# Kernel tuning notes

Measured on AMD Instinct MI355X. Metric: run time of the kernel, lower is better.

Reference implementation:

```python
import jax, jax.numpy as jnp
import numpy as np

G = 60            # 60x60 macroblock MV grid (960px / 16px blocks)
IMAGE_SIZE = 960.0
LN_EPS = 1e-5


def layer_norm(x, g, b):
    mu = jnp.mean(x, -1, keepdims=True)
    var = jnp.var(x, -1, keepdims=True)
    return (x - mu) / jnp.sqrt(var + LN_EPS) * g + b


def setup_inputs() -> dict:
    key = jax.random.key(0)
    ks = iter(jax.random.split(key, 40))
    nk = lambda: next(ks)
    N = 4096
    MVF, BED, H = 64, 32, 128
    D_IN = MVF + BED  # 96

    def lin(out_d, in_d):
        w = jax.random.normal(nk(), (out_d, in_d), jnp.float32) * np.float32(1.0 / np.sqrt(in_d))
        b = jnp.zeros((out_d,), jnp.float32)
        return w, b

    motion_vectors = jax.random.normal(nk(), (1, 2, G, G), jnp.float32)
    xy = jax.random.uniform(nk(), (N, 2), jnp.float32, 0.0, 800.0)
    wh = jax.random.uniform(nk(), (N, 2), jnp.float32, 16.0, 160.0)
    boxes = jnp.concatenate([xy, jnp.clip(xy + wh, 0.0, IMAGE_SIZE)], axis=-1)

    inp = {"motion_vectors": motion_vectors, "boxes": boxes}
    # stats projection: 6 stats (mean/std/range x 2 channels) -> MVF
    inp["W_stats"], inp["b_stats"] = lin(MVF, 6)
    inp["g_stats"] = jnp.ones((MVF,), jnp.float32); inp["be_stats"] = jnp.zeros((MVF,), jnp.float32)
    # box coordinate encoder
    inp["W_b1"], inp["b_b1"] = lin(BED, 4)
    inp["g_b1"] = jnp.ones((BED,), jnp.float32); inp["be_b1"] = jnp.zeros((BED,), jnp.float32)
    inp["W_b2"], inp["b_b2"] = lin(BED, BED)
    inp["g_b2"] = jnp.ones((BED,), jnp.float32); inp["be_b2"] = jnp.zeros((BED,), jnp.float32)
    # single-layer LSTM (torch gate order i,f,g,o)
    inp["W_ih"] = jax.random.normal(nk(), (4 * H, D_IN), jnp.float32) * np.float32(1.0 / np.sqrt(D_IN))
    inp["W_hh"] = jax.random.normal(nk(), (4 * H, H), jnp.float32) * np.float32(1.0 / np.sqrt(H))
    inp["b_ih"] = jnp.zeros((4 * H,), jnp.float32)
    inp["b_hh"] = jnp.zeros((4 * H,), jnp.float32)
    # heads
    inp["W_p1"], inp["b_p1"] = lin(H // 2, H); inp["W_p2"], inp["b_p2"] = lin(2, H // 2)
    inp["W_s1"], inp["b_s1"] = lin(H // 2, H); inp["W_s2"], inp["b_s2"] = lin(2, H // 2)
    inp["W_c1"], inp["b_c1"] = lin(H // 2, H); inp["W_c2"], inp["b_c2"] = lin(1, H // 2)
    return inp


def _box_motion_stats(motion_vectors, boxes_norm):
    # motion_vectors: [1,2,G,G]; boxes_norm: [N,4] in [0,1]
    mvf = motion_vectors[0].reshape(2, G * G)  # [2, 3600]
    x1 = jnp.clip(jnp.floor(boxes_norm[:, 0] * G).astype(jnp.int32), 0, G - 1)
    y1 = jnp.clip(jnp.floor(boxes_norm[:, 1] * G).astype(jnp.int32), 0, G - 1)
    x2 = jnp.clip(jnp.ceil(boxes_norm[:, 2] * G).astype(jnp.int32), x1 + 1, G)
    y2 = jnp.clip(jnp.ceil(boxes_norm[:, 3] * G).astype(jnp.int32), y1 + 1, G)
    idx = jnp.arange(G)
    mx = (idx[None, :] >= x1[:, None]) & (idx[None, :] < x2[:, None])  # [N,G]
    my = (idx[None, :] >= y1[:, None]) & (idx[None, :] < y2[:, None])  # [N,G]
    mask = (my[:, :, None] & mx[:, None, :]).reshape(-1, G * G).astype(mvf.dtype)  # [N,3600]
    cnt = mask.sum(-1, keepdims=True)  # >= 1 by construction
    s = jnp.einsum('nc,kc->nk', mask, mvf)          # [N,2]
    sq = jnp.einsum('nc,kc->nk', mask, mvf * mvf)   # [N,2]
    mean = s / cnt
    std = jnp.sqrt(jnp.clip(sq / cnt - mean * mean, 0.0))
    big = jnp.asarray(1e30, mvf.dtype)
    hi = jnp.where(mask[:, None, :] > 0, mvf[None], -big).max(-1)  # [N,2]
    lo = jnp.where(mask[:, None, :] > 0, mvf[None], big).min(-1)   # [N,2]
    return jnp.concatenate([mean, std, hi - lo], axis=-1)  # [N,6]


def reference(motion_vectors, boxes,
              W_stats, b_stats, g_stats, be_stats,
              W_b1, b_b1, g_b1, be_b1, W_b2, b_b2, g_b2, be_b2,
              W_ih, W_hh, b_ih, b_hh,
              W_p1, b_p1, W_p2, b_p2, W_s1, b_s1, W_s2, b_s2, W_c1, b_c1, W_c2, b_c2):
    N = boxes.shape[0]
    H = W_hh.shape[1]
    boxes_norm = jnp.clip(boxes / IMAGE_SIZE, 0.0, 1.0)

    # per-box motion feature (BoxAlignedMotionEncoder: gather region -> mean/std/range -> proj)
    stats = _box_motion_stats(motion_vectors, boxes_norm)
    mv_feat = jax.nn.relu(layer_norm(stats @ W_stats.T + b_stats, g_stats, be_stats))  # [N,64]

    # box coordinate encoder (dropout = identity in eval)
    h1 = jax.nn.relu(layer_norm(boxes_norm @ W_b1.T + b_b1, g_b1, be_b1))
    box_feat = jax.nn.relu(layer_norm(h1 @ W_b2.T + b_b2, g_b2, be_b2))  # [N,32]

    x = jnp.concatenate([mv_feat, box_feat], axis=-1)  # [N,96]

    # single-step LSTM, zero initial state, torch gate order i,f,g,o
    h0 = jnp.zeros((N, H), x.dtype)
    c0 = jnp.zeros((N, H), x.dtype)
    gates = x @ W_ih.T + h0 @ W_hh.T + b_ih + b_hh
    i, f, g, o = jnp.split(gates, 4, axis=-1)
    c = jax.nn.sigmoid(f) * c0 + jax.nn.sigmoid(i) * jnp.tanh(g)
    h = jax.nn.sigmoid(o) * jnp.tanh(c)  # [N,128]

    pos = jax.nn.relu(h @ W_p1.T + b_p1) @ W_p2.T + b_p2    # [N,2]
    size = jax.nn.relu(h @ W_s1.T + b_s1) @ W_s2.T + b_s2   # [N,2]
    conf = jax.nn.relu(h @ W_c1.T + b_c1) @ W_c2.T + b_c2   # [N,1]
    confidences = jax.nn.sigmoid(conf[:, 0])

    # box update: shift center by deltas, scale w/h by exp(size_deltas)
    x1, y1, x2, y2 = boxes[:, 0], boxes[:, 1], boxes[:, 2], boxes[:, 3]
    cx, cy = (x1 + x2) * 0.5, (y1 + y2) * 0.5
    w, hgt = x2 - x1, y2 - y1
    ncx, ncy = cx + pos[:, 0], cy + pos[:, 1]
    nw, nh = w * jnp.exp(size[:, 0]), hgt * jnp.exp(size[:, 1])
    pred = jnp.stack([ncx - nw * 0.5, ncy - nh * 0.5, ncx + nw * 0.5, ncy + nh * 0.5], axis=-1)
    return jnp.concatenate([pred, confidences[:, None]], axis=-1)  # [N,5]
```

## Files before the change

kernel.cpp:

```cpp
#include <hip/hip_runtime.h>
#include <math.h>

#define GRID_G 60
#define GRID_GG 3600
#define BPB 8

__device__ __forceinline__ float wred32sum(float v){
  #pragma unroll
  for (int m = 16; m; m >>= 1) v += __shfl_xor(v, m, 32);
  return v;
}
__device__ __forceinline__ float wred32max(float v){
  #pragma unroll
  for (int m = 16; m; m >>= 1) v = fmaxf(v, __shfl_xor(v, m, 32));
  return v;
}
__device__ __forceinline__ float wred32min(float v){
  #pragma unroll
  for (int m = 16; m; m >>= 1) v = fminf(v, __shfl_xor(v, m, 32));
  return v;
}
__device__ __forceinline__ float frcp(float x){ return __builtin_amdgcn_rcpf(x); }
__device__ __forceinline__ float fsig(float x){ return frcp(1.0f + __expf(-x)); }
__device__ __forceinline__ float ftanh(float x){ return 1.0f - 2.0f*frcp(1.0f + __expf(2.0f*x)); }

__global__ __launch_bounds__(256) void transpose_kernel(
    const float* __restrict__ W_ih,
    const float* __restrict__ W_p1, const float* __restrict__ W_s1,
    const float* __restrict__ W_c1,
    float* __restrict__ wt_ih, float* __restrict__ wt_h)
{
  const int i4 = blockIdx.x * 256 + threadIdx.x;
  if (i4 < 9216) {
    const int e = i4 * 4;
    const int k = e / 384, r0 = e % 384;
    float4 v;
    {
      const int r = r0;     const int row = (r < 128) ? r : r + 128; v.x = W_ih[row*96 + k];
    }
    { const int r = r0 + 1; const int row = (r < 128) ? r : r + 128; v.y = W_ih[row*96 + k]; }
    { const int r = r0 + 2; const int row = (r < 128) ? r : r + 128; v.z = W_ih[row*96 + k]; }
    { const int r = r0 + 3; const int row = (r < 128) ? r : r + 128; v.w = W_ih[row*96 + k]; }
    ((float4*)wt_ih)[i4] = v;
  } else if (i4 < 9216 + 6144) {
    const int j4 = i4 - 9216;
    const int e = j4 * 4;
    const int k = e / 192, r0 = e % 192;
    const float* W = (r0 < 64) ? W_p1 : (r0 < 128) ? W_s1 : W_c1;
    float4 v;
    v.x = W[((r0    ) & 63) * 128 + k];
    v.y = W[((r0 + 1) & 63) * 128 + k];
    v.z = W[((r0 + 2) & 63) * 128 + k];
    v.w = W[((r0 + 3) & 63) * 128 + k];
    ((float4*)wt_h)[j4] = v;
  }
}

__global__ __launch_bounds__(256) void tracker_kernel(
    const float* __restrict__ mv,
    const float* __restrict__ boxes,
    const float* __restrict__ W_stats, const float* __restrict__ b_stats,
    const float* __restrict__ g_stats, const float* __restrict__ be_stats,
    const float* __restrict__ W_b1,  const float* __restrict__ b_b1,
    const float* __restrict__ g_b1,  const float* __restrict__ be_b1,
    const float* __restrict__ W_b2,  const float* __restrict__ b_b2,
    const float* __restrict__ g_b2,  const float* __restrict__ be_b2,
    const float* __restrict__ wt_ih,
    const float* __restrict__ b_ih,  const float* __restrict__ b_hh,
    const float* __restrict__ wt_h,
    const float* __restrict__ b_p1,  const float* __restrict__ W_p2, const float* __restrict__ b_p2,
    const float* __restrict__ b_s1,  const float* __restrict__ W_s2, const float* __restrict__ b_s2,
    const float* __restrict__ b_c1,  const float* __restrict__ W_c2, const float* __restrict__ b_c2,
    float* __restrict__ out, int N)
{
  __shared__ __align__(16) float x_lds[BPB][96];
  __shared__ __align__(16) float sA[BPB][384];
  __shared__ __align__(16) float sB[BPB][384];
  __shared__ __align__(16) float h_lds[BPB][128];
  __shared__ __align__(16) float h1_lds[BPB][32];
  __shared__ float u_lds[3*BPB][65];
  __shared__ float res_lds[BPB][5];

  const int tid  = threadIdx.x;
  const int base = blockIdx.x * BPB;

  {
    const int b   = tid >> 5;
    const int l32 = tid & 31;
    int gb = base + b; if (gb >= N) gb = N - 1;
    const float4 bx = ((const float4*)boxes)[gb];
    const float bn0 = fminf(fmaxf(bx.x * (1.0f/960.0f), 0.f), 1.f);
    const float bn1 = fminf(fmaxf(bx.y * (1.0f/960.0f), 0.f), 1.f);
    const float bn2 = fminf(fmaxf(bx.z * (1.0f/960.0f), 0.f), 1.f);
    const float bn3 = fminf(fmaxf(bx.w * (1.0f/960.0f), 0.f), 1.f);

    int x1 = (int)floorf(bn0 * 60.f); x1 = min(max(x1, 0), 59);
    int y1 = (int)floorf(bn1 * 60.f); y1 = min(max(y1, 0), 59);
    int x2 = (int)ceilf (bn2 * 60.f); x2 = min(max(x2, x1 + 1), 60);
    int y2 = (int)ceilf (bn3 * 60.f); y2 = min(max(y2, y1 + 1), 60);
    const int w = x2 - x1, hh = y2 - y1;
    const int cnt = w * hh;
    const float rw = 1.0f / (float)w;

    float s0=0.f, s1=0.f, q0=0.f, q1=0.f;
    float hi0=-1e30f, hi1=-1e30f, lo0=1e30f, lo1=1e30f;
    for (int c = l32; c < cnt; c += 32) {
      const int yy = (int)(((float)c + 0.5f) * rw);
      const int xx = c - yy * w;
      const int idx = (y1 + yy) * GRID_G + (x1 + xx);
      const float m0 = mv[idx];
      const float m1 = mv[GRID_GG + idx];
      s0 += m0; q0 += m0*m0; hi0 = fmaxf(hi0, m0); lo0 = fminf(lo0, m0);
      s1 += m1; q1 += m1*m1; hi1 = fmaxf(hi1, m1); lo1 = fminf(lo1, m1);
    }
    s0 = wred32sum(s0); q0 = wred32sum(q0); hi0 = wred32max(hi0); lo0 = wred32min(lo0);
    s1 = wred32sum(s1); q1 = wred32sum(q1); hi1 = wred32max(hi1); lo1 = wred32min(lo1);
    const float inv = frcp((float)cnt);
    float st[6];
    st[0] = s0 * inv;
    st[1] = s1 * inv;
    st[2] = sqrtf(fmaxf(q0 * inv - st[0]*st[0], 0.f));
    st[3] = sqrtf(fmaxf(q1 * inv - st[1]*st[1], 0.f));
    st[4] = hi0 - lo0;
    st[5] = hi1 - lo1;

    {
      const float* Wr0 = W_stats + l32 * 6;
      const float* Wr1 = W_stats + (l32 + 32) * 6;
      float v0 = b_stats[l32], v1 = b_stats[l32 + 32];
      #pragma unroll
      for (int k = 0; k < 6; ++k) { v0 = fmaf(st[k], Wr0[k], v0); v1 = fmaf(st[k], Wr1[k], v1); }
      const float mu  = wred32sum(v0 + v1) * (1.0f/64.0f);
      const float var = wred32sum(v0*v0 + v1*v1) * (1.0f/64.0f) - mu*mu;
      const float rs  = rsqrtf(var + 1e-5f);
      x_lds[b][l32     ] = fmaxf((v0-mu)*rs*g_stats[l32     ] + be_stats[l32     ], 0.f);
      x_lds[b][l32 + 32] = fmaxf((v1-mu)*rs*g_stats[l32 + 32] + be_stats[l32 + 32], 0.f);
    }

    {
      const float* Wr = W_b1 + l32 * 4;
      const float v = b_b1[l32] + bn0*Wr[0] + bn1*Wr[1] + bn2*Wr[2] + bn3*Wr[3];
      const float mu  = wred32sum(v)   * (1.0f/32.0f);
      const float var = wred32sum(v*v) * (1.0f/32.0f) - mu*mu;
      h1_lds[b][l32] = fmaxf((v - mu) * rsqrtf(var + 1e-5f) * g_b1[l32] + be_b1[l32], 0.f);
    }
    __threadfence_block();

    {
      const float* Wr = W_b2 + l32 * 32;
      float v = b_b2[l32];
      #pragma unroll
      for (int kk = 0; kk < 8; ++kk) {
        const float4 hv = *(const float4*)(&h1_lds[b][kk * 4]);
        const float4 wv = *(const float4*)(&Wr[kk * 4]);
        v = fmaf(wv.x,hv.x, fmaf(wv.y,hv.y, fmaf(wv.z,hv.z, fmaf(wv.w,hv.w, v))));
      }
      const float mu  = wred32sum(v)   * (1.0f/32.0f);
      const float var = wred32sum(v*v) * (1.0f/32.0f) - mu*mu;
      x_lds[b][64 + l32] = fmaxf((v - mu) * rsqrtf(var + 1e-5f) * g_b2[l32] + be_b2[l32], 0.f);
    }
  }
  __syncthreads();

  if (tid < 192) {
    const int q = (tid < 96) ? tid : tid - 96;
    const int s = (tid < 96) ? 0 : 1;
    float acc[4][BPB];
    #pragma unroll
    for (int j = 0; j < 4; ++j)
      #pragma unroll
      for (int b = 0; b < BPB; ++b) acc[j][b] = 0.f;
    const float4* WT = (const float4*)wt_ih;
    const int k0 = s * 48;
    #pragma unroll 2
    for (int k4 = 0; k4 < 12; ++k4) {
      const int kb = k0 + 4*k4;
      const float4 wv0 = WT[(size_t)(kb    ) * 96 + q];
      const float4 wv1 = WT[(size_t)(kb + 1) * 96 + q];
      const float4 wv2 = WT[(size_t)(kb + 2) * 96 + q];
      const float4 wv3 = WT[(size_t)(kb + 3) * 96 + q];
      #pragma unroll
      for (int b = 0; b < BPB; ++b) {
        const float4 xv = *(const float4*)(&x_lds[b][kb]);
        acc[0][b] = fmaf(wv0.x, xv.x, fmaf(wv1.x, xv.y, fmaf(wv2.x, xv.z, fmaf(wv3.x, xv.w, acc[0][b]))));
        acc[1][b] = fmaf(wv0.y, xv.x, fmaf(wv1.y, xv.y, fmaf(wv2.y, xv.z, fmaf(wv3.y, xv.w, acc[1][b]))));
        acc[2][b] = fmaf(wv0.z, xv.x, fmaf(wv1.z, xv.y, fmaf(wv2.z, xv.z, fmaf(wv3.z, xv.w, acc[2][b]))));
        acc[3][b] = fmaf(wv0.w, xv.x, fmaf(wv1.w, xv.y, fmaf(wv2.w, xv.z, fmaf(wv3.w, xv.w, acc[3][b]))));
      }
    }
    float* dst = (s == 0) ? &sA[0][0] : &sB[0][0];
    #pragma unroll
    for (int b = 0; b < BPB; ++b) {
      float4 v; v.x = acc[0][b]; v.y = acc[1][b]; v.z = acc[2][b]; v.w = acc[3][b];
      *(float4*)(dst + b * 384 + 4 * q) = v;
    }
  }
  __syncthreads();

  {
    const int j    = tid & 127;
    const int half = tid >> 7;
    const float bi = b_ih[j      ] + b_hh[j      ];
    const float bg = b_ih[j + 256] + b_hh[j + 256];
    const float bo = b_ih[j + 384] + b_hh[j + 384];
    #pragma unroll
    for (int bb = 0; bb < 4; ++bb) {
      const int b = half * 4 + bb;
      const float ai = sA[b][j      ] + sB[b][j      ] + bi;
      const float ag = sA[b][128 + j] + sB[b][128 + j] + bg;
      const float ao = sA[b][256 + j] + sB[b][256 + j] + bo;
      const float c  = fsig(ai) * ftanh(ag);
      h_lds[b][j] = fsig(ao) * ftanh(c);
    }
  }
  __syncthreads();

  if (tid < 192) {
    const int q48 = tid % 48;
    const int s4  = tid / 48;
    float acc[4][BPB];
    #pragma unroll
    for (int j = 0; j < 4; ++j)
      #pragma unroll
      for (int b = 0; b < BPB; ++b) acc[j][b] = 0.f;
    const float4* WT = (const float4*)wt_h;
    const int k0 = s4 * 32;
    #pragma unroll 2
    for (int k4 = 0; k4 < 8; ++k4) {
      const int kb = k0 + 4*k4;
      const float4 wv0 = WT[(size_t)(kb    ) * 48 + q48];
      const float4 wv1 = WT[(size_t)(kb + 1) * 48 + q48];
      const float4 wv2 = WT[(size_t)(kb + 2) * 48 + q48];
      const float4 wv3 = WT[(size_t)(kb + 3) * 48 + q48];
      #pragma unroll
      for (int b = 0; b < BPB; ++b) {
        const float4 hv = *(const float4*)(&h_lds[b][kb]);
        acc[0][b] = fmaf(wv0.x, hv.x, fmaf(wv1.x, hv.y, fmaf(wv2.x, hv.z, fmaf(wv3.x, hv.w, acc[0][b]))));
        acc[1][b] = fmaf(wv0.y, hv.x, fmaf(wv1.y, hv.y, fmaf(wv2.y, hv.z, fmaf(wv3.y, hv.w, acc[1][b]))));
        acc[2][b] = fmaf(wv0.z, hv.x, fmaf(wv1.z, hv.y, fmaf(wv2.z, hv.z, fmaf(wv3.z, hv.w, acc[2][b]))));
        acc[3][b] = fmaf(wv0.w, hv.x, fmaf(wv1.w, hv.y, fmaf(wv2.w, hv.z, fmaf(wv3.w, hv.w, acc[3][b]))));
      }
    }
    float* dst = (s4 < 2) ? &sA[0][0] : &sB[0][0];
    const int off = (s4 & 1) * 192;
    #pragma unroll
    for (int b = 0; b < BPB; ++b) {
      float4 v; v.x = acc[0][b]; v.y = acc[1][b]; v.z = acc[2][b]; v.w = acc[3][b];
      *(float4*)(dst + b * 384 + off + 4 * q48) = v;
    }
  }
  __syncthreads();

  {
    #pragma unroll
    for (int i = 0; i < 6; ++i) {
      const int idx = tid + 256 * i;
      const int b = idx / 192;
      const int r = idx - b * 192;
      const int head = r >> 6, brow = r & 63;
      const float bias = ((head == 0) ? b_p1 : (head == 1) ? b_s1 : b_c1)[brow];
      const float v = sA[b][r] + sA[b][192 + r] + sB[b][r] + sB[b][192 + r] + bias;
      u_lds[head * BPB + b][brow] = fmaxf(v, 0.f);
    }
  }
  __syncthreads();

  if (tid < BPB * 5) {
    const int b = tid / 5, o = tid % 5;
    const int head = (o < 2) ? 0 : (o < 4) ? 1 : 2;
    const float* W2; float bias;
    if      (o == 0) { W2 = W_p2;      bias = b_p2[0]; }
    else if (o == 1) { W2 = W_p2 + 64; bias = b_p2[1]; }
    else if (o == 2) { W2 = W_s2;      bias = b_s2[0]; }
    else if (o == 3) { W2 = W_s2 + 64; bias = b_s2[1]; }
    else             { W2 = W_c2;      bias = b_c2[0]; }
    const float* ur = u_lds[head * BPB + b];
    float a0 = bias, a1 = 0.f, a2 = 0.f, a3 = 0.f;
    #pragma unroll 4
    for (int k = 0; k < 64; k += 4) {
      a0 = fmaf(ur[k  ], W2[k  ], a0);
      a1 = fmaf(ur[k+1], W2[k+1], a1);
      a2 = fmaf(ur[k+2], W2[k+2], a2);
      a3 = fmaf(ur[k+3], W2[k+3], a3);
    }
    res_lds[b][o] = (a0 + a1) + (a2 + a3);
  }
  __syncthreads();

  if (tid < BPB) {
    const int gb = base + tid;
    if (gb < N) {
      const float4 bx = ((const float4*)boxes)[gb];
      const float cx = (bx.x + bx.z) * 0.5f;
      const float cy = (bx.y + bx.w) * 0.5f;
      const float w  = bx.z - bx.x;
      const float hh = bx.w - bx.y;
      const float ncx = cx + res_lds[tid][0];
      const float ncy = cy + res_lds[tid][1];
      const float nw  = w  * __expf(res_lds[tid][2]);
      const float nh  = hh * __expf(res_lds[tid][3]);
      const float cf  = fsig(res_lds[tid][4]);
      float* op = out + (size_t)gb * 5;
      op[0] = ncx - nw * 0.5f;
      op[1] = ncy - nh * 0.5f;
      op[2] = ncx + nw * 0.5f;
      op[3] = ncy + nh * 0.5f;
      op[4] = cf;
    }
  }
}

extern "C" void kernel_launch(void* const* d_in, const int* in_sizes, int n_in,
                              void* d_out, int out_size, void* d_ws, size_t ws_size,
                              hipStream_t stream) {
  (void)n_in; (void)out_size; (void)ws_size;
  const float* mv       = (const float*)d_in[0];
  const float* boxes    = (const float*)d_in[1];
  const float* W_stats  = (const float*)d_in[2];
  const float* b_stats  = (const float*)d_in[3];
  const float* g_stats  = (const float*)d_in[4];
  const float* be_stats = (const float*)d_in[5];
  const float* W_b1     = (const float*)d_in[6];
  const float* b_b1     = (const float*)d_in[7];
  const float* g_b1     = (const float*)d_in[8];
  const float* be_b1    = (const float*)d_in[9];
  const float* W_b2     = (const float*)d_in[10];
  const float* b_b2     = (const float*)d_in[11];
  const float* g_b2     = (const float*)d_in[12];
  const float* be_b2    = (const float*)d_in[13];
  const float* W_ih     = (const float*)d_in[14];
  const float* b_ih     = (const float*)d_in[16];
  const float* b_hh     = (const float*)d_in[17];
  const float* W_p1     = (const float*)d_in[18];
  const float* b_p1     = (const float*)d_in[19];
  const float* W_p2     = (const float*)d_in[20];
  const float* b_p2     = (const float*)d_in[21];
  const float* W_s1     = (const float*)d_in[22];
  const float* b_s1     = (const float*)d_in[23];
  const float* W_s2     = (const float*)d_in[24];
  const float* b_s2     = (const float*)d_in[25];
  const float* W_c1     = (const float*)d_in[26];
  const float* b_c1     = (const float*)d_in[27];
  const float* W_c2     = (const float*)d_in[28];
  const float* b_c2     = (const float*)d_in[29];

  float* wt_ih = (float*)d_ws;
  float* wt_h  = wt_ih + 96 * 384;

  transpose_kernel<<<60, 256, 0, stream>>>(W_ih, W_p1, W_s1, W_c1, wt_ih, wt_h);

  const int N = in_sizes[1] / 4;
  const int grid = (N + BPB - 1) / BPB;
  tracker_kernel<<<grid, 256, 0, stream>>>(
      mv, boxes,
      W_stats, b_stats, g_stats, be_stats,
      W_b1, b_b1, g_b1, be_b1,
      W_b2, b_b2, g_b2, be_b2,
      wt_ih, b_ih, b_hh,
      wt_h,
      b_p1, W_p2, b_p2,
      b_s1, W_s2, b_s2,
      b_c1, W_c2, b_c2,
      (float*)d_out, N);
}
```

Measured before the change: 131.5 us.

## Double block size to 512 threads with finer split-K partial sums

Each block now uses 512 threads, giving one full 64-lane wavefront per box in the motion-stat and encoder stage, and wave64 reductions replace the 32-lane ones. The LSTM input matmul and the head first layers split K into four and eight slices, writing partials to a four-buffer LDS array that later stages sum. This is meant to shorten per-thread serial work and raise parallelism per block. In exchange it uses more LDS per block, adds partial-sum reads, and half the lanes sit idle in the 32-wide encoder steps.

```diff
diff --git a/kernel.cpp b/kernel.cpp
--- a/kernel.cpp
+++ b/kernel.cpp
@@ -5,19 +5,19 @@
 #define GRID_GG 3600
 #define BPB 8
 
-__device__ __forceinline__ float wred32sum(float v){
+__device__ __forceinline__ float wredsum(float v){
   #pragma unroll
-  for (int m = 16; m; m >>= 1) v += __shfl_xor(v, m, 32);
+  for (int m = 32; m; m >>= 1) v += __shfl_xor(v, m, 64);
   return v;
 }
-__device__ __forceinline__ float wred32max(float v){
+__device__ __forceinline__ float wredmax(float v){
   #pragma unroll
-  for (int m = 16; m; m >>= 1) v = fmaxf(v, __shfl_xor(v, m, 32));
+  for (int m = 32; m; m >>= 1) v = fmaxf(v, __shfl_xor(v, m, 64));
   return v;
 }
-__device__ __forceinline__ float wred32min(float v){
+__device__ __forceinline__ float wredmin(float v){
   #pragma unroll
-  for (int m = 16; m; m >>= 1) v = fminf(v, __shfl_xor(v, m, 32));
+  for (int m = 32; m; m >>= 1) v = fminf(v, __shfl_xor(v, m, 64));
   return v;
 }
 __device__ __forceinline__ float frcp(float x){ return __builtin_amdgcn_rcpf(x); }
@@ -35,9 +35,7 @@
     const int e = i4 * 4;
     const int k = e / 384, r0 = e % 384;
     float4 v;
-    {
-      const int r = r0;     const int row = (r < 128) ? r : r + 128; v.x = W_ih[row*96 + k];
-    }
+    { const int r = r0;     const int row = (r < 128) ? r : r + 128; v.x = W_ih[row*96 + k]; }
     { const int r = r0 + 1; const int row = (r < 128) ? r : r + 128; v.y = W_ih[row*96 + k]; }
     { const int r = r0 + 2; const int row = (r < 128) ? r : r + 128; v.z = W_ih[row*96 + k]; }
     { const int r = r0 + 3; const int row = (r < 128) ? r : r + 128; v.w = W_ih[row*96 + k]; }
@@ -56,7 +54,7 @@
   }
 }
 
-__global__ __launch_bounds__(256) void tracker_kernel(
+__global__ __launch_bounds__(512, 4) void tracker_kernel(
     const float* __restrict__ mv,
     const float* __restrict__ boxes,
     const float* __restrict__ W_stats, const float* __restrict__ b_stats,
@@ -74,8 +72,7 @@
     float* __restrict__ out, int N)
 {
   __shared__ __align__(16) float x_lds[BPB][96];
-  __shared__ __align__(16) float sA[BPB][384];
-  __shared__ __align__(16) float sB[BPB][384];
+  __shared__ __align__(16) float sP[4][BPB][384];
   __shared__ __align__(16) float h_lds[BPB][128];
   __shared__ __align__(16) float h1_lds[BPB][32];
   __shared__ float u_lds[3*BPB][65];
@@ -85,8 +82,9 @@
   const int base = blockIdx.x * BPB;
 
   {
-    const int b   = tid >> 5;
-    const int l32 = tid & 31;
+    const int b    = tid >> 6;
+    const int lane = tid & 63;
+    const int l32  = lane & 31;
     int gb = base + b; if (gb >= N) gb = N - 1;
     const float4 bx = ((const float4*)boxes)[gb];
     const float bn0 = fminf(fmaxf(bx.x * (1.0f/960.0f), 0.f), 1.f);
@@ -104,7 +102,7 @@
 
     float s0=0.f, s1=0.f, q0=0.f, q1=0.f;
     float hi0=-1e30f, hi1=-1e30f, lo0=1e30f, lo1=1e30f;
-    for (int c = l32; c < cnt; c += 32) {
+    for (int c = lane; c < cnt; c += 64) {
       const int yy = (int)(((float)c + 0.5f) * rw);
       const int xx = c - yy * w;
       const int idx = (y1 + yy) * GRID_G + (x1 + xx);
@@ -113,8 +111,8 @@
       s0 += m0; q0 += m0*m0; hi0 = fmaxf(hi0, m0); lo0 = fminf(lo0, m0);
       s1 += m1; q1 += m1*m1; hi1 = fmaxf(hi1, m1); lo1 = fminf(lo1, m1);
     }
-    s0 = wred32sum(s0); q0 = wred32sum(q0); hi0 = wred32max(hi0); lo0 = wred32min(lo0);
-    s1 = wred32sum(s1); q1 = wred32sum(q1); hi1 = wred32max(hi1); lo1 = wred32min(lo1);
+    s0 = wredsum(s0); q0 = wredsum(q0); hi0 = wredmax(hi0); lo0 = wredmin(lo0);
+    s1 = wredsum(s1); q1 = wredsum(q1); hi1 = wredmax(hi1); lo1 = wredmin(lo1);
     const float inv = frcp((float)cnt);
     float st[6];
     st[0] = s0 * inv;
@@ -125,24 +123,24 @@
     st[5] = hi1 - lo1;
 
     {
-      const float* Wr0 = W_stats + l32 * 6;
-      const float* Wr1 = W_stats + (l32 + 32) * 6;
-      float v0 = b_stats[l32], v1 = b_stats[l32 + 32];
-      #pragma unroll
-      for (int k = 0; k < 6; ++k) { v0 = fmaf(st[k], Wr0[k], v0); v1 = fmaf(st[k], Wr1[k], v1); }
-      const float mu  = wred32sum(v0 + v1) * (1.0f/64.0f);
-      const float var = wred32sum(v0*v0 + v1*v1) * (1.0f/64.0f) - mu*mu;
-      const float rs  = rsqrtf(var + 1e-5f);
-      x_lds[b][l32     ] = fmaxf((v0-mu)*rs*g_stats[l32     ] + be_stats[l32     ], 0.f);
-      x_lds[b][l32 + 32] = fmaxf((v1-mu)*rs*g_stats[l32 + 32] + be_stats[l32 + 32], 0.f);
+      const float* Wr = W_stats + lane * 6;
+      float v = b_stats[lane];
+      #pragma unroll
+      for (int k = 0; k < 6; ++k) v = fmaf(st[k], Wr[k], v);
+      const float mu  = wredsum(v)   * (1.0f/64.0f);
+      const float var = wredsum(v*v) * (1.0f/64.0f) - mu*mu;
+      x_lds[b][lane] = fmaxf((v - mu) * rsqrtf(var + 1e-5f) * g_stats[lane] + be_stats[lane], 0.f);
     }
 
     {
       const float* Wr = W_b1 + l32 * 4;
       const float v = b_b1[l32] + bn0*Wr[0] + bn1*Wr[1] + bn2*Wr[2] + bn3*Wr[3];
-      const float mu  = wred32sum(v)   * (1.0f/32.0f);
-      const float var = wred32sum(v*v) * (1.0f/32.0f) - mu*mu;
-      h1_lds[b][l32] = fmaxf((v - mu) * rsqrtf(var + 1e-5f) * g_b1[l32] + be_b1[l32], 0.f);
+      const float cv  = (lane < 32) ? v   : 0.f;
+      const float cq  = (lane < 32) ? v*v : 0.f;
+      const float mu  = wredsum(cv) * (1.0f/32.0f);
+      const float var = wredsum(cq) * (1.0f/32.0f) - mu*mu;
+      const float h1v = fmaxf((v - mu) * rsqrtf(var + 1e-5f) * g_b1[l32] + be_b1[l32], 0.f);
+      if (lane < 32) h1_lds[b][l32] = h1v;
     }
     __threadfence_block();
 
@@ -155,25 +153,28 @@
         const float4 wv = *(const float4*)(&Wr[kk * 4]);
         v = fmaf(wv.x,hv.x, fmaf(wv.y,hv.y, fmaf(wv.z,hv.z, fmaf(wv.w,hv.w, v))));
       }
-      const float mu  = wred32sum(v)   * (1.0f/32.0f);
-      const float var = wred32sum(v*v) * (1.0f/32.0f) - mu*mu;
-      x_lds[b][64 + l32] = fmaxf((v - mu) * rsqrtf(var + 1e-5f) * g_b2[l32] + be_b2[l32], 0.f);
-    }
-  }
-  __syncthreads();
-
-  if (tid < 192) {
-    const int q = (tid < 96) ? tid : tid - 96;
-    const int s = (tid < 96) ? 0 : 1;
+      const float cv  = (lane < 32) ? v   : 0.f;
+      const float cq  = (lane < 32) ? v*v : 0.f;
+      const float mu  = wredsum(cv) * (1.0f/32.0f);
+      const float var = wredsum(cq) * (1.0f/32.0f) - mu*mu;
+      const float y = fmaxf((v - mu) * rsqrtf(var + 1e-5f) * g_b2[l32] + be_b2[l32], 0.f);
+      if (lane < 32) x_lds[b][64 + l32] = y;
+    }
+  }
+  __syncthreads();
+
+  if (tid < 384) {
+    const int q = tid % 96;
+    const int s = tid / 96;
+    const int k0 = s * 24;
     float acc[4][BPB];
     #pragma unroll
     for (int j = 0; j < 4; ++j)
       #pragma unroll
       for (int b = 0; b < BPB; ++b) acc[j][b] = 0.f;
     const float4* WT = (const float4*)wt_ih;
-    const int k0 = s * 48;
     #pragma unroll 2
-    for (int k4 = 0; k4 < 12; ++k4) {
+    for (int k4 = 0; k4 < 6; ++k4) {
       const int kb = k0 + 4*k4;
       const float4 wv0 = WT[(size_t)(kb    ) * 96 + q];
       const float4 wv1 = WT[(size_t)(kb + 1) * 96 + q];
@@ -188,45 +189,44 @@
         acc[3][b] = fmaf(wv0.w, xv.x, fmaf(wv1.w, xv.y, fmaf(wv2.w, xv.z, fmaf(wv3.w, xv.w, acc[3][b]))));
       }
     }
-    float* dst = (s == 0) ? &sA[0][0] : &sB[0][0];
     #pragma unroll
     for (int b = 0; b < BPB; ++b) {
       float4 v; v.x = acc[0][b]; v.y = acc[1][b]; v.z = acc[2][b]; v.w = acc[3][b];
-      *(float4*)(dst + b * 384 + 4 * q) = v;
+      *(float4*)(&sP[s][b][4*q]) = v;
     }
   }
   __syncthreads();
 
   {
-    const int j    = tid & 127;
-    const int half = tid >> 7;
+    const int j  = tid & 127;
+    const int g2 = tid >> 7;
     const float bi = b_ih[j      ] + b_hh[j      ];
     const float bg = b_ih[j + 256] + b_hh[j + 256];
     const float bo = b_ih[j + 384] + b_hh[j + 384];
     #pragma unroll
-    for (int bb = 0; bb < 4; ++bb) {
-      const int b = half * 4 + bb;
-      const float ai = sA[b][j      ] + sB[b][j      ] + bi;
-      const float ag = sA[b][128 + j] + sB[b][128 + j] + bg;
-      const float ao = sA[b][256 + j] + sB[b][256 + j] + bo;
+    for (int bb = 0; bb < 2; ++bb) {
+      const int b = g2 * 2 + bb;
+      const float ai = sP[0][b][j      ] + sP[1][b][j      ] + sP[2][b][j      ] + sP[3][b][j      ] + bi;
+      const float ag = sP[0][b][128 + j] + sP[1][b][128 + j] + sP[2][b][128 + j] + sP[3][b][128 + j] + bg;
+      const float ao = sP[0][b][256 + j] + sP[1][b][256 + j] + sP[2][b][256 + j] + sP[3][b][256 + j] + bo;
       const float c  = fsig(ai) * ftanh(ag);
       h_lds[b][j] = fsig(ao) * ftanh(c);
     }
   }
   __syncthreads();
 
-  if (tid < 192) {
+  if (tid < 384) {
     const int q48 = tid % 48;
-    const int s4  = tid / 48;
+    const int s8  = tid / 48;
+    const int k0  = s8 * 16;
     float acc[4][BPB];
     #pragma unroll
     for (int j = 0; j < 4; ++j)
       #pragma unroll
       for (int b = 0; b < BPB; ++b) acc[j][b] = 0.f;
     const float4* WT = (const float4*)wt_h;
-    const int k0 = s4 * 32;
     #pragma unroll 2
-    for (int k4 = 0; k4 < 8; ++k4) {
+    for (int k4 = 0; k4 < 4; ++k4) {
       const int kb = k0 + 4*k4;
       const float4 wv0 = WT[(size_t)(kb    ) * 48 + q48];
       const float4 wv1 = WT[(size_t)(kb + 1) * 48 + q48];
@@ -241,25 +241,27 @@
         acc[3][b] = fmaf(wv0.w, hv.x, fmaf(wv1.w, hv.y, fmaf(wv2.w, hv.z, fmaf(wv3.w, hv.w, acc[3][b]))));
       }
     }
-    float* dst = (s4 < 2) ? &sA[0][0] : &sB[0][0];
-    const int off = (s4 & 1) * 192;
+    const int buf = s8 >> 1;
+    const int off = (s8 & 1) * 192;
     #pragma unroll
     for (int b = 0; b < BPB; ++b) {
       float4 v; v.x = acc[0][b]; v.y = acc[1][b]; v.z = acc[2][b]; v.w = acc[3][b];
-      *(float4*)(dst + b * 384 + off + 4 * q48) = v;
+      *(float4*)(&sP[buf][b][off + 4 * q48]) = v;
     }
   }
   __syncthreads();
 
   {
     #pragma unroll
-    for (int i = 0; i < 6; ++i) {
-      const int idx = tid + 256 * i;
+    for (int i = 0; i < 3; ++i) {
+      const int idx = tid + 512 * i;
       const int b = idx / 192;
       const int r = idx - b * 192;
       const int head = r >> 6, brow = r & 63;
       const float bias = ((head == 0) ? b_p1 : (head == 1) ? b_s1 : b_c1)[brow];
-      const float v = sA[b][r] + sA[b][192 + r] + sB[b][r] + sB[b][192 + r] + bias;
+      float v = bias;
+      #pragma unroll
+      for (int p = 0; p < 8; ++p) v += sP[p >> 1][b][(p & 1) * 192 + r];
       u_lds[head * BPB + b][brow] = fmaxf(v, 0.f);
     }
   }
@@ -351,7 +353,7 @@
 
   const int N = in_sizes[1] / 4;
   const int grid = (N + BPB - 1) / BPB;
-  tracker_kernel<<<grid, 256, 0, stream>>>(
+  tracker_kernel<<<grid, 512, 0, stream>>>(
       mv, boxes,
       W_stats, b_stats, g_stats, be_stats,
       W_b1, b_b1, g_b1, be_b1,
```

After: 134.9 us. 1.03x slower.

## Store transposed LSTM and head weights as packed bf16, widen per-thread output tile

Applied to the files above, without the earlier changes.

The transpose kernel now converts the gathered LSTM input weights and head first-layer weights to bf16 and packs two per 32-bit word, halving weight bytes read by every block. Each thread in the two matmul stages now computes 8 outputs instead of 4, with the K dimension split 4 or 8 ways, and partial sums go into a single 4-slice LDS buffer that is reduced later. This cuts global/L2 weight traffic per block at the cost of bf16 rounding error in the weights, more accumulator registers (64 floats), and extra LDS reduction work.

```diff
diff --git a/kernel.cpp b/kernel.cpp
--- a/kernel.cpp
+++ b/kernel.cpp
@@ -24,35 +24,36 @@
 __device__ __forceinline__ float fsig(float x){ return frcp(1.0f + __expf(-x)); }
 __device__ __forceinline__ float ftanh(float x){ return 1.0f - 2.0f*frcp(1.0f + __expf(2.0f*x)); }
 
+__device__ __forceinline__ unsigned short f2bf(float x){
+  unsigned int u = __float_as_uint(x);
+  return (unsigned short)((u + 0x7fffu + ((u >> 16) & 1u)) >> 16);
+}
+__device__ __forceinline__ float bf_lo(unsigned int u){ return __uint_as_float(u << 16); }
+__device__ __forceinline__ float bf_hi(unsigned int u){ return __uint_as_float(u & 0xffff0000u); }
+
 __global__ __launch_bounds__(256) void transpose_kernel(
     const float* __restrict__ W_ih,
     const float* __restrict__ W_p1, const float* __restrict__ W_s1,
     const float* __restrict__ W_c1,
-    float* __restrict__ wt_ih, float* __restrict__ wt_h)
+    unsigned int* __restrict__ wt_ih2, unsigned int* __restrict__ wt_h2)
 {
-  const int i4 = blockIdx.x * 256 + threadIdx.x;
-  if (i4 < 9216) {
-    const int e = i4 * 4;
+  const int i = blockIdx.x * 256 + threadIdx.x;
+  if (i < 18432) {
+    const int e = i * 2;
     const int k = e / 384, r0 = e % 384;
-    float4 v;
-    {
-      const int r = r0;     const int row = (r < 128) ? r : r + 128; v.x = W_ih[row*96 + k];
-    }
-    { const int r = r0 + 1; const int row = (r < 128) ? r : r + 128; v.y = W_ih[row*96 + k]; }
-    { const int r = r0 + 2; const int row = (r < 128) ? r : r + 128; v.z = W_ih[row*96 + k]; }
-    { const int r = r0 + 3; const int row = (r < 128) ? r : r + 128; v.w = W_ih[row*96 + k]; }
-    ((float4*)wt_ih)[i4] = v;
-  } else if (i4 < 9216 + 6144) {
-    const int j4 = i4 - 9216;
-    const int e = j4 * 4;
+    const int row0 = (r0     < 128) ? r0     : r0 + 128;
+    const int row1 = (r0 + 1 < 128) ? r0 + 1 : r0 + 1 + 128;
+    const unsigned int lo = f2bf(W_ih[row0 * 96 + k]);
+    const unsigned int hi = f2bf(W_ih[row1 * 96 + k]);
+    wt_ih2[i] = lo | (hi << 16);
+  } else if (i < 18432 + 12288) {
+    const int j = i - 18432;
+    const int e = j * 2;
     const int k = e / 192, r0 = e % 192;
     const float* W = (r0 < 64) ? W_p1 : (r0 < 128) ? W_s1 : W_c1;
-    float4 v;
-    v.x = W[((r0    ) & 63) * 128 + k];
-    v.y = W[((r0 + 1) & 63) * 128 + k];
-    v.z = W[((r0 + 2) & 63) * 128 + k];
-    v.w = W[((r0 + 3) & 63) * 128 + k];
-    ((float4*)wt_h)[j4] = v;
+    const unsigned int lo = f2bf(W[((r0    ) & 63) * 128 + k]);
+    const unsigned int hi = f2bf(W[((r0 + 1) & 63) * 128 + k]);
+    wt_h2[j] = lo | (hi << 16);
   }
 }
 
@@ -65,17 +66,16 @@
     const float* __restrict__ g_b1,  const float* __restrict__ be_b1,
     const float* __restrict__ W_b2,  const float* __restrict__ b_b2,
     const float* __restrict__ g_b2,  const float* __restrict__ be_b2,
-    const float* __restrict__ wt_ih,
+    const unsigned int* __restrict__ wt_ih2,
     const float* __restrict__ b_ih,  const float* __restrict__ b_hh,
-    const float* __restrict__ wt_h,
+    const unsigned int* __restrict__ wt_h2,
     const float* __restrict__ b_p1,  const float* __restrict__ W_p2, const float* __restrict__ b_p2,
     const float* __restrict__ b_s1,  const float* __restrict__ W_s2, const float* __restrict__ b_s2,
     const float* __restrict__ b_c1,  const float* __restrict__ W_c2, const float* __restrict__ b_c2,
     float* __restrict__ out, int N)
 {
   __shared__ __align__(16) float x_lds[BPB][96];
-  __shared__ __align__(16) float sA[BPB][384];
-  __shared__ __align__(16) float sB[BPB][384];
+  __shared__ __align__(16) float sP[4][BPB][384];
   __shared__ __align__(16) float h_lds[BPB][128];
   __shared__ __align__(16) float h1_lds[BPB][32];
   __shared__ float u_lds[3*BPB][65];
@@ -163,52 +163,66 @@
   __syncthreads();
 
   if (tid < 192) {
-    const int q = (tid < 96) ? tid : tid - 96;
-    const int s = (tid < 96) ? 0 : 1;
-    float acc[4][BPB];
-    #pragma unroll
-    for (int j = 0; j < 4; ++j)
+    const int o = tid % 48;
+    const int s = tid / 48;
+    const int k0 = s * 24;
+    float acc[8][BPB];
+    #pragma unroll
+    for (int j = 0; j < 8; ++j)
       #pragma unroll
       for (int b = 0; b < BPB; ++b) acc[j][b] = 0.f;
-    const float4* WT = (const float4*)wt_ih;
-    const int k0 = s * 48;
     #pragma unroll 2
-    for (int k4 = 0; k4 < 12; ++k4) {
+    for (int k4 = 0; k4 < 6; ++k4) {
       const int kb = k0 + 4*k4;
-      const float4 wv0 = WT[(size_t)(kb    ) * 96 + q];
-      const float4 wv1 = WT[(size_t)(kb + 1) * 96 + q];
-      const float4 wv2 = WT[(size_t)(kb + 2) * 96 + q];
-      const float4 wv3 = WT[(size_t)(kb + 3) * 96 + q];
-      #pragma unroll
-      for (int b = 0; b < BPB; ++b) {
-        const float4 xv = *(const float4*)(&x_lds[b][kb]);
-        acc[0][b] = fmaf(wv0.x, xv.x, fmaf(wv1.x, xv.y, fmaf(wv2.x, xv.z, fmaf(wv3.x, xv.w, acc[0][b]))));
-        acc[1][b] = fmaf(wv0.y, xv.x, fmaf(wv1.y, xv.y, fmaf(wv2.y, xv.z, fmaf(wv3.y, xv.w, acc[1][b]))));
-        acc[2][b] = fmaf(wv0.z, xv.x, fmaf(wv1.z, xv.y, fmaf(wv2.z, xv.z, fmaf(wv3.z, xv.w, acc[2][b]))));
-        acc[3][b] = fmaf(wv0.w, xv.x, fmaf(wv1.w, xv.y, fmaf(wv2.w, xv.z, fmaf(wv3.w, xv.w, acc[3][b]))));
+      uint4 W[4];
+      #pragma unroll
+      for (int kk = 0; kk < 4; ++kk)
+        W[kk] = *(const uint4*)(wt_ih2 + ((size_t)(kb + kk) * 384 + 8*o) / 2);
+      float4 xv[BPB];
+      #pragma unroll
+      for (int b = 0; b < BPB; ++b) xv[b] = *(const float4*)(&x_lds[b][kb]);
+      #pragma unroll
+      for (int kk = 0; kk < 4; ++kk) {
+        const float w0 = bf_lo(W[kk].x), w1 = bf_hi(W[kk].x);
+        const float w2 = bf_lo(W[kk].y), w3 = bf_hi(W[kk].y);
+        const float w4 = bf_lo(W[kk].z), w5 = bf_hi(W[kk].z);
+        const float w6 = bf_lo(W[kk].w), w7 = bf_hi(W[kk].w);
+        #pragma unroll
+        for (int b = 0; b < BPB; ++b) {
+          const float xc = (kk == 0) ? xv[b].x : (kk == 1) ? xv[b].y : (kk == 2) ? xv[b].z : xv[b].w;
+          acc[0][b] = fmaf(w0, xc, acc[0][b]);
+          acc[1][b] = fmaf(w1, xc, acc[1][b]);
+          acc[2][b] = fmaf(w2, xc, acc[2][b]);
+          acc[3][b] = fmaf(w3, xc, acc[3][b]);
+          acc[4][b] = fmaf(w4, xc, acc[4][b]);
+          acc[5][b] = fmaf(w5, xc, acc[5][b]);
+          acc[6][b] = fmaf(w6, xc, acc[6][b]);
+          acc[7][b] = fmaf(w7, xc, acc[7][b]);
+        }
       }
     }
-    float* dst = (s == 0) ? &sA[0][0] : &sB[0][0];
     #pragma unroll
     for (int b = 0; b < BPB; ++b) {
-      float4 v; v.x = acc[0][b]; v.y = acc[1][b]; v.z = acc[2][b]; v.w = acc[3][b];
-      *(float4*)(dst + b * 384 + 4 * q) = v;
+      float4 v0; v0.x = acc[0][b]; v0.y = acc[1][b]; v0.z = acc[2][b]; v0.w = acc[3][b];
+      float4 v1; v1.x = acc[4][b]; v1.y = acc[5][b]; v1.z = acc[6][b]; v1.w = acc[7][b];
+      *(float4*)(&sP[s][b][8*o    ]) = v0;
+      *(float4*)(&sP[s][b][8*o + 4]) = v1;
     }
   }
   __syncthreads();
 
   {
-    const int j    = tid & 127;
-    const int half = tid >> 7;
+    const int j  = tid & 127;
+    const int g2 = tid >> 7;
     const float bi = b_ih[j      ] + b_hh[j      ];
     const float bg = b_ih[j + 256] + b_hh[j + 256];
     const float bo = b_ih[j + 384] + b_hh[j + 384];
     #pragma unroll
     for (int bb = 0; bb < 4; ++bb) {
-      const int b = half * 4 + bb;
-      const float ai = sA[b][j      ] + sB[b][j      ] + bi;
-      const float ag = sA[b][128 + j] + sB[b][128 + j] + bg;
-      const float ao = sA[b][256 + j] + sB[b][256 + j] + bo;
+      const int b = g2 * 4 + bb;
+      const float ai = sP[0][b][j      ] + sP[1][b][j      ] + sP[2][b][j      ] + sP[3][b][j      ] + bi;
+      const float ag = sP[0][b][128 + j] + sP[1][b][128 + j] + sP[2][b][128 + j] + sP[3][b][128 + j] + bg;
+      const float ao = sP[0][b][256 + j] + sP[1][b][256 + j] + sP[2][b][256 + j] + sP[3][b][256 + j] + bo;
       const float c  = fsig(ai) * ftanh(ag);
       h_lds[b][j] = fsig(ao) * ftanh(c);
     }
@@ -216,37 +230,52 @@
   __syncthreads();
 
   if (tid < 192) {
-    const int q48 = tid % 48;
-    const int s4  = tid / 48;
-    float acc[4][BPB];
-    #pragma unroll
-    for (int j = 0; j < 4; ++j)
+    const int o  = tid % 24;
+    const int s8 = tid / 24;
+    const int k0 = s8 * 16;
+    float acc[8][BPB];
+    #pragma unroll
+    for (int j = 0; j < 8; ++j)
       #pragma unroll
       for (int b = 0; b < BPB; ++b) acc[j][b] = 0.f;
-    const float4* WT = (const float4*)wt_h;
-    const int k0 = s4 * 32;
     #pragma unroll 2
-    for (int k4 = 0; k4 < 8; ++k4) {
+    for (int k4 = 0; k4 < 4; ++k4) {
       const int kb = k0 + 4*k4;
-      const float4 wv0 = WT[(size_t)(kb    ) * 48 + q48];
-      const float4 wv1 = WT[(size_t)(kb + 1) * 48 + q48];
-      const float4 wv2 = WT[(size_t)(kb + 2) * 48 + q48];
-      const float4 wv3 = WT[(size_t)(kb + 3) * 48 + q48];
-      #pragma unroll
-      for (int b = 0; b < BPB; ++b) {
-        const float4 hv = *(const float4*)(&h_lds[b][kb]);
-        acc[0][b] = fmaf(wv0.x, hv.x, fmaf(wv1.x, hv.y, fmaf(wv2.x, hv.z, fmaf(wv3.x, hv.w, acc[0][b]))));
-        acc[1][b] = fmaf(wv0.y, hv.x, fmaf(wv1.y, hv.y, fmaf(wv2.y, hv.z, fmaf(wv3.y, hv.w, acc[1][b]))));
-        acc[2][b] = fmaf(wv0.z, hv.x, fmaf(wv1.z, hv.y, fmaf(wv2.z, hv.z, fmaf(wv3.z, hv.w, acc[2][b]))));
-        acc[3][b] = fmaf(wv0.w, hv.x, fmaf(wv1.w, hv.y, fmaf(wv2.w, hv.z, fmaf(wv3.w, hv.w, acc[3][b]))));
+      uint4 W[4];
+      #pragma unroll
+      for (int kk = 0; kk < 4; ++kk)
+        W[kk] = *(const uint4*)(wt_h2 + ((size_t)(kb + kk) * 192 + 8*o) / 2);
+      float4 hv[BPB];
+      #pragma unroll
+      for (int b = 0; b < BPB; ++b) hv[b] = *(const float4*)(&h_lds[b][kb]);
+      #pragma unroll
+      for (int kk = 0; kk < 4; ++kk) {
+        const float w0 = bf_lo(W[kk].x), w1 = bf_hi(W[kk].x);
+        const float w2 = bf_lo(W[kk].y), w3 = bf_hi(W[kk].y);
+        const float w4 = bf_lo(W[kk].z), w5 = bf_hi(W[kk].z);
+        const float w6 = bf_lo(W[kk].w), w7 = bf_hi(W[kk].w);
+        #pragma unroll
+        for (int b = 0; b < BPB; ++b) {
+          const float hc = (kk == 0) ? hv[b].x : (kk == 1) ? hv[b].y : (kk == 2) ? hv[b].z : hv[b].w;
+          acc[0][b] = fmaf(w0, hc, acc[0][b]);
+          acc[1][b] = fmaf(w1, hc, acc[1][b]);
+          acc[2][b] = fmaf(w2, hc, acc[2][b]);
+          acc[3][b] = fmaf(w3, hc, acc[3][b]);
+          acc[4][b] = fmaf(w4, hc, acc[4][b]);
+          acc[5][b] = fmaf(w5, hc, acc[5][b]);
+          acc[6][b] = fmaf(w6, hc, acc[6][b]);
+          acc[7][b] = fmaf(w7, hc, acc[7][b]);
+        }
       }
     }
-    float* dst = (s4 < 2) ? &sA[0][0] : &sB[0][0];
-    const int off = (s4 & 1) * 192;
+    const int buf = s8 >> 1;
+    const int off = (s8 & 1) * 192;
     #pragma unroll
     for (int b = 0; b < BPB; ++b) {
-      float4 v; v.x = acc[0][b]; v.y = acc[1][b]; v.z = acc[2][b]; v.w = acc[3][b];
-      *(float4*)(dst + b * 384 + off + 4 * q48) = v;
+      float4 v0; v0.x = acc[0][b]; v0.y = acc[1][b]; v0.z = acc[2][b]; v0.w = acc[3][b];
+      float4 v1; v1.x = acc[4][b]; v1.y = acc[5][b]; v1.z = acc[6][b]; v1.w = acc[7][b];
+      *(float4*)(&sP[buf][b][off + 8*o    ]) = v0;
+      *(float4*)(&sP[buf][b][off + 8*o + 4]) = v1;
     }
   }
   __syncthreads();
@@ -259,7 +288,9 @@
       const int r = idx - b * 192;
       const int head = r >> 6, brow = r & 63;
       const float bias = ((head == 0) ? b_p1 : (head == 1) ? b_s1 : b_c1)[brow];
-      const float v = sA[b][r] + sA[b][192 + r] + sB[b][r] + sB[b][192 + r] + bias;
+      float v = bias;
+      #pragma unroll
+      for (int p = 0; p < 8; ++p) v += sP[p >> 1][b][(p & 1) * 192 + r];
       u_lds[head * BPB + b][brow] = fmaxf(v, 0.f);
     }
   }
@@ -344,10 +375,10 @@
   const float* W_c2     = (const float*)d_in[28];
   const float* b_c2     = (const float*)d_in[29];
 
-  float* wt_ih = (float*)d_ws;
-  float* wt_h  = wt_ih + 96 * 384;
-
-  transpose_kernel<<<60, 256, 0, stream>>>(W_ih, W_p1, W_s1, W_c1, wt_ih, wt_h);
+  unsigned int* wt_ih2 = (unsigned int*)d_ws;
+  unsigned int* wt_h2  = wt_ih2 + 18432;
+
+  transpose_kernel<<<120, 256, 0, stream>>>(W_ih, W_p1, W_s1, W_c1, wt_ih2, wt_h2);
 
   const int N = in_sizes[1] / 4;
   const int grid = (N + BPB - 1) / BPB;
@@ -356,8 +387,8 @@
       W_stats, b_stats, g_stats, be_stats,
       W_b1, b_b1, g_b1, be_b1,
       W_b2, b_b2, g_b2, be_b2,
-      wt_ih, b_ih, b_hh,
-      wt_h,
+      wt_ih2, b_ih, b_hh,
+      wt_h2,
       b_p1, W_p2, b_p2,
       b_s1, W_s2, b_s2,
       b_c1, W_c2, b_c2,
```

Measured after the change: 132.7 us. About the same (+0.9%).
